# Performance work log

Hardware: AMD Instinct MI355X
Metric: run time of the kernel (lower is better)

The kernel has to match this reference:

```python
import jax, jax.numpy as jnp
import numpy as np
import math

B, S, HID, NH, INTER, L = 8, 512, 768, 12, 3072, 4
DH = HID // NH
EPS = 1e-12


def setup_inputs() -> dict:
    key = jax.random.key(0)
    ks = jax.random.split(key, 12)
    s = 0.02
    hidden_states = jax.random.normal(ks[0], (B, S, HID), jnp.float32)
    lengths = jax.random.randint(ks[1], (B,), S // 2, S + 1)
    attention_mask = (jnp.arange(S)[None, :] < lengths[:, None]).astype(jnp.float32)
    return dict(
        hidden_states=hidden_states,
        attention_mask=attention_mask,
        Wqkv_w=jax.random.normal(ks[2], (L, 3 * HID, HID), jnp.float32) * s,
        Wqkv_b=jnp.zeros((L, 3 * HID), jnp.float32),
        attn_out_w=jax.random.normal(ks[3], (L, HID, HID), jnp.float32) * s,
        attn_out_b=jnp.zeros((L, HID), jnp.float32),
        ln1_g=jnp.ones((L, HID), jnp.float32),
        ln1_b=jnp.zeros((L, HID), jnp.float32),
        glu_w=jax.random.normal(ks[4], (L, 2 * INTER, HID), jnp.float32) * s,
        wo_w=jax.random.normal(ks[5], (L, HID, INTER), jnp.float32) * s,
        wo_b=jnp.zeros((L, HID), jnp.float32),
        ln2_g=jnp.ones((L, HID), jnp.float32),
        ln2_b=jnp.zeros((L, HID), jnp.float32),
        r1=1.0 + 0.1 * jax.random.normal(ks[6], (L, NH, 1, 1), jnp.float32),
        r2=1.0 + 0.1 * jax.random.normal(ks[7], (L, NH, 1, 1), jnp.float32),
        r3=1.0 + 0.1 * jax.random.normal(ks[8], (L, NH, 1, 1), jnp.float32),
    )


def _ln(x, g, b):
    mu = x.mean(-1, keepdims=True)
    var = ((x - mu) ** 2).mean(-1, keepdims=True)
    return (x - mu) / jnp.sqrt(var + EPS) * g + b


def _forward(hidden_states, attention_mask, Wqkv_w, Wqkv_b, attn_out_w, attn_out_b,
             ln1_g, ln1_b, glu_w, wo_w, wo_b, ln2_g, ln2_b, r1, r2, r3):
    mask = attention_mask  # [B,S] float, 1=valid
    pos = jnp.arange(S)
    rel = jnp.abs(pos[None, :] - pos[:, None]).astype(jnp.float32)  # [S,S]
    rel_pos = rel > 0
    attn_bias = (1.0 - mask)[:, None, None, :] * -10000.0  # [B,1,1,S]
    # unpad_input <-> zero invalid rows of padded tensor
    h = hidden_states * mask[:, :, None]
    for l in range(L):
        c1 = jnp.clip(r1[l], 1e-7)  # [NH,1,1]
        c2 = jnp.clip(r2[l], 1e-7)
        c3 = jnp.clip(r3[l], 1e-7)
        relp = jnp.where(rel_pos, rel, 1.0) ** c3  # [NH,S,S], safe pow at |i-j|=0
        relp = jnp.where(rel_pos, relp, 0.0)
        kb = -c1 * jnp.log1p(c2 * relp)  # kerple bias [NH,S,S]
        bias = attn_bias + kb[None]  # [B,NH,S,S]
        # qkv on valid tokens only (pad_input reinserts zeros)
        qkv = (h @ Wqkv_w[l].T + Wqkv_b[l]) * mask[:, :, None]
        qkv = qkv.reshape(B, S, 3, NH, DH)
        q = qkv[:, :, 0].transpose(0, 2, 1, 3)  # [B,NH,S,DH]
        k = qkv[:, :, 1].transpose(0, 2, 1, 3)
        v = qkv[:, :, 2].transpose(0, 2, 1, 3)
        scores = jnp.einsum('bhqd,bhkd->bhqk', q, k) / math.sqrt(DH) + bias
        probs = jax.nn.softmax(scores, axis=-1)
        attn = jnp.einsum('bhqk,bhkd->bhqd', probs, v)
        attn = attn.transpose(0, 2, 1, 3).reshape(B, S, HID)
        ao = _ln(attn @ attn_out_w[l].T + attn_out_b[l] + h, ln1_g[l], ln1_b[l])
        ao = ao * mask[:, :, None]
        g = ao @ glu_w[l].T  # [B,S,2*INTER]
        x = jax.nn.gelu(g[..., :INTER], approximate=False) * g[..., INTER:]
        h = _ln(x @ wo_w[l].T + wo_b[l] + ao, ln2_g[l], ln2_b[l])
        h = h * mask[:, :, None]
    return h


def reference(hidden_states, attention_mask, Wqkv_w, Wqkv_b, attn_out_w, attn_out_b,
              ln1_g, ln1_b, glu_w, wo_w, wo_b, ln2_g, ln2_b, r1, r2, r3):
    return _forward(hidden_states, attention_mask, Wqkv_w, Wqkv_b, attn_out_w,
                    attn_out_b, ln1_g, ln1_b, glu_w, wo_w, wo_b, ln2_g, ln2_b,
                    r1, r2, r3)
```

## Files before the change

kernel.cpp:

```cpp
#include <hip/hip_runtime.h>
#include <hip/hip_bf16.h>
#include <math.h>

#define BQ 8
#define SQ 512
#define HID 768
#define NH 12
#define DH 64
#define INTER 3072
#define NL 4
#define M_TOK (BQ*SQ)

typedef unsigned short ushort_t;
typedef __attribute__((ext_vector_type(8))) short bf16x8;
typedef __attribute__((ext_vector_type(8))) unsigned short u16x8;
typedef __attribute__((ext_vector_type(4))) float f32x4;

__device__ __forceinline__ float bf2f(ushort_t u) {
  union { float f; unsigned int i; } v; v.i = ((unsigned int)u) << 16; return v.f;
}
__device__ __forceinline__ ushort_t f2bf(float f) {
  __hip_bfloat16 h = __float2bfloat16(f);
  return *reinterpret_cast<ushort_t*>(&h);
}

__device__ __forceinline__ void gload_lds16(const ushort_t* g, ushort_t* l) {
  __builtin_amdgcn_global_load_lds(
      (const __attribute__((address_space(1))) void*)g,
      (__attribute__((address_space(3))) void*)l, 16, 0, 0);
}

__global__ __launch_bounds__(256) void prep_kernel(
    const float* __restrict__ hidden, const float* __restrict__ amask,
    float* __restrict__ maskf, float* __restrict__ maskbias,
    float* __restrict__ h, ushort_t* __restrict__ hb)
{
  int i = blockIdx.x * 256 + threadIdx.x;
  if (i < M_TOK * HID) {
    float m = amask[i / HID];
    float v = hidden[i] * m;
    h[i] = v;
    hb[i] = f2bf(v);
    if (i < M_TOK) {
      maskf[i] = amask[i];
      maskbias[i] = (1.0f - amask[i]) * (-10000.0f);
    }
  }
}

__global__ void kerple_all_kernel(const float* __restrict__ r1,
                                  const float* __restrict__ r2,
                                  const float* __restrict__ r3,
                                  float* __restrict__ kbt_all)
{
  int lh = blockIdx.x;
  int d  = threadIdx.x;
  float c1 = fmaxf(r1[lh], 1e-7f);
  float c2 = fmaxf(r2[lh], 1e-7f);
  float c3 = fmaxf(r3[lh], 1e-7f);
  float v = 0.0f;
  if (d > 0) v = -c1 * log1pf(c2 * powf((float)d, c3));
  kbt_all[lh * SQ + d] = v;
}

#define WS0 (3*HID*HID)
#define WS1 (HID*HID)
#define WS2 (2*INTER*HID)
#define WS3 (HID*INTER)
#define WTOT (WS0+WS1+WS2+WS3)

__global__ __launch_bounds__(256) void wcast_layer_kernel(
    const float* __restrict__ w0, const float* __restrict__ w1,
    const float* __restrict__ w2, const float* __restrict__ w3,
    ushort_t* __restrict__ dst)
{
  int i = (blockIdx.x * 256 + threadIdx.x) * 4;
  if (i >= WTOT) return;
  const float* src; int off;
  if (i < WS0)                { src = w0; off = i; }
  else if (i < WS0+WS1)       { src = w1; off = i - WS0; }
  else if (i < WS0+WS1+WS2)   { src = w2; off = i - WS0 - WS1; }
  else                        { src = w3; off = i - WS0 - WS1 - WS2; }
  float4 v = *reinterpret_cast<const float4*>(src + off);
  ushort4 o;
  o.x = f2bf(v.x); o.y = f2bf(v.y); o.z = f2bf(v.z); o.w = f2bf(v.w);
  *reinterpret_cast<ushort4*>(dst + i) = o;
}

template<int NB, int EPI>
__global__ __launch_bounds__(256, 2) void mfma_gemm(
    const ushort_t* __restrict__ A, const ushort_t* __restrict__ B0p,
    const ushort_t* __restrict__ B1p, const float* __restrict__ bias,
    const float* __restrict__ rowscale, ushort_t* __restrict__ Cb,
    int N, int K)
{
  __shared__ ushort_t As_[128 * 64];
  __shared__ ushort_t Bs_[NB][128 * 64];
  int tid = threadIdx.x;
  int lane = tid & 63, w = tid >> 6;
  int wr = w >> 1, wc = w & 1;
  int bn = blockIdx.x, bm = blockIdx.y;

  f32x4 acc[NB][4][4];
#pragma unroll
  for (int p = 0; p < NB; ++p)
#pragma unroll
    for (int m = 0; m < 4; ++m)
#pragma unroll
      for (int n = 0; n < 4; ++n) acc[p][m][n] = (f32x4){0.f, 0.f, 0.f, 0.f};

  int sr[4], sc[4], so[4];
#pragma unroll
  for (int i = 0; i < 4; ++i) {
    int o = w * 4096 + i * 1024 + lane * 16;
    sr[i] = o >> 7;
    int cl = (o >> 4) & 7;
    sc[i] = cl ^ (sr[i] & 7);
    so[i] = (w * 4096 + i * 1024) >> 1;
  }
  const ushort_t* Arow  = A   + (size_t)bm * 128 * K;
  const ushort_t* Brow0 = B0p + (size_t)bn * 128 * K;
  const ushort_t* Brow1 = (NB == 2) ? (B1p + (size_t)bn * 128 * K) : nullptr;

  int aoff[4][2], boff[4][2];
#pragma unroll
  for (int m = 0; m < 4; ++m)
#pragma unroll
    for (int kh = 0; kh < 2; ++kh) {
      int ra = wr * 64 + m * 16 + (lane & 15);
      int rb = wc * 64 + m * 16 + (lane & 15);
      int ch = (kh * 4 + (lane >> 4)) ^ (lane & 7);
      aoff[m][kh] = ra * 64 + ch * 8;
      boff[m][kh] = rb * 64 + ch * 8;
    }

  for (int k0 = 0; k0 < K; k0 += 64) {
#pragma unroll
    for (int i = 0; i < 4; ++i)
      gload_lds16(Arow + (size_t)sr[i] * K + k0 + sc[i] * 8, As_ + so[i]);
#pragma unroll
    for (int i = 0; i < 4; ++i)
      gload_lds16(Brow0 + (size_t)sr[i] * K + k0 + sc[i] * 8, &Bs_[0][so[i]]);
    if constexpr (NB == 2) {
#pragma unroll
      for (int i = 0; i < 4; ++i)
        gload_lds16(Brow1 + (size_t)sr[i] * K + k0 + sc[i] * 8, &Bs_[1][so[i]]);
    }
    __syncthreads();
#pragma unroll
    for (int kh = 0; kh < 2; ++kh) {
      bf16x8 af[4], bf_[4];
#pragma unroll
      for (int m = 0; m < 4; ++m) af[m] = *(const bf16x8*)(As_ + aoff[m][kh]);
#pragma unroll
      for (int n = 0; n < 4; ++n) bf_[n] = *(const bf16x8*)(&Bs_[0][boff[n][kh]]);
#pragma unroll
      for (int m = 0; m < 4; ++m)
#pragma unroll
        for (int n = 0; n < 4; ++n)
          acc[0][m][n] = __builtin_amdgcn_mfma_f32_16x16x32_bf16(
              af[m], bf_[n], acc[0][m][n], 0, 0, 0);
      if constexpr (NB == 2) {
        bf16x8 bg[4];
#pragma unroll
        for (int n = 0; n < 4; ++n) bg[n] = *(const bf16x8*)(&Bs_[1][boff[n][kh]]);
#pragma unroll
        for (int m = 0; m < 4; ++m)
#pragma unroll
          for (int n = 0; n < 4; ++n)
            acc[1][m][n] = __builtin_amdgcn_mfma_f32_16x16x32_bf16(
                af[m], bg[n], acc[1][m][n], 0, 0, 0);
      }
    }
    __syncthreads();
  }

  int r0 = bm * 128 + wr * 64, c0 = bn * 128 + wc * 64;
#pragma unroll
  for (int m = 0; m < 4; ++m)
#pragma unroll
    for (int n = 0; n < 4; ++n) {
      int col  = c0 + n * 16 + (lane & 15);
      int rowb = r0 + m * 16 + (lane >> 4) * 4;
      if constexpr (EPI == 0) {
        float bv = bias ? bias[col] : 0.0f;
#pragma unroll
        for (int j = 0; j < 4; ++j)
          Cb[(size_t)(rowb + j) * N + col] = f2bf(acc[0][m][n][j] + bv);
      } else if constexpr (EPI == 1) {
#pragma unroll
        for (int j = 0; j < 4; ++j) {
          float va = acc[0][m][n][j];
          float vb = acc[1][m][n][j];
          float ge = 0.5f * va * (1.0f + erff(va * 0.70710678118654752440f));
          Cb[(size_t)(rowb + j) * N + col] = f2bf(ge * vb);
        }
      } else {
        float bv = bias ? bias[col] : 0.0f;
#pragma unroll
        for (int j = 0; j < 4; ++j) {
          float v = (acc[0][m][n][j] + bv) * rowscale[rowb + j];
          Cb[(size_t)(rowb + j) * N + col] = f2bf(v);
        }
      }
    }
}

__global__ __launch_bounds__(256) void attn_mfma(
    const ushort_t* __restrict__ qkvb, const float* __restrict__ kbt,
    const float* __restrict__ maskbias, ushort_t* __restrict__ attnb)
{
  __shared__ ushort_t Ks[64 * 64];
  __shared__ ushort_t Vt[64 * 64];
  __shared__ ushort_t Ps[64 * 64];
  __shared__ float    kbs[SQ];
  __shared__ float    mbs[SQ];

  int tid  = threadIdx.x;
  int lane = tid & 63, w = tid >> 6;
  int g = lane >> 4, r = lane & 15;
  int bid = blockIdx.x;
  int qt = bid & 7;
  int hh = (bid >> 3) % NH;
  int b  = bid / (8 * NH);
  int q0 = qt * 64;

  for (int i = tid; i < SQ; i += 256) {
    kbs[i] = kbt[hh * SQ + i];
    mbs[i] = maskbias[b * SQ + i];
  }

  bf16x8 qf[2];
  {
    const ushort_t* qsrc = qkvb + (size_t)(b * SQ + q0 + w * 16 + r) * (3 * HID)
                         + hh * DH + g * 8;
    qf[0] = *(const bf16x8*)(qsrc);
    qf[1] = *(const bf16x8*)(qsrc + 32);
  }

  float m_run[4], l_run[4];
  f32x4 oacc[4];
#pragma unroll
  for (int j = 0; j < 4; ++j) { m_run[j] = -1e30f; l_run[j] = 0.f; }
#pragma unroll
  for (int nd = 0; nd < 4; ++nd) oacc[nd] = (f32x4){0.f, 0.f, 0.f, 0.f};

  int k2 = (tid & 31) * 2, dg = tid >> 5;

  for (int kc = 0; kc < 8; ++kc) {
    __syncthreads();
#pragma unroll
    for (int ii = 0; ii < 2; ++ii) {
      int row = (w * 2 + ii) * 8 + (lane >> 3);
      int c   = lane & 7;
      const ushort_t* src = qkvb + (size_t)(b * SQ + kc * 64 + row) * (3 * HID)
                          + HID + hh * DH + ((c ^ (row & 7)) * 8);
      gload_lds16(src, Ks + (w * 2 + ii) * 512 + lane * 8);
    }
    {
      const ushort_t* v0 = qkvb + (size_t)(b * SQ + kc * 64 + k2) * (3 * HID)
                         + 2 * HID + hh * DH + dg * 8;
      const ushort_t* v1 = v0 + 3 * HID;
      u16x8 a = *(const u16x8*)v0;
      u16x8 c = *(const u16x8*)v1;
#pragma unroll
      for (int u = 0; u < 8; ++u) {
        int d = dg * 8 + u;
        int addr = d * 64 + (((k2 >> 3) ^ (d & 7)) * 8) + (k2 & 7);
        ushort2 pr; pr.x = (ushort_t)a[u]; pr.y = (ushort_t)c[u];
        *(ushort2*)(Vt + addr) = pr;
      }
    }
    __syncthreads();

    f32x4 sacc[4];
#pragma unroll
    for (int n = 0; n < 4; ++n) sacc[n] = (f32x4){0.f, 0.f, 0.f, 0.f};
    __builtin_amdgcn_s_setprio(1);
#pragma unroll
    for (int kh = 0; kh < 2; ++kh) {
#pragma unroll
      for (int n = 0; n < 4; ++n) {
        bf16x8 kf = *(const bf16x8*)(Ks + (n * 16 + r) * 64
                                     + (((g + kh * 4) ^ (r & 7)) * 8));
        sacc[n] = __builtin_amdgcn_mfma_f32_16x16x32_bf16(qf[kh], kf, sacc[n], 0, 0, 0);
      }
    }
    __builtin_amdgcn_s_setprio(0);

    float sval[4][4], mx[4];
#pragma unroll
    for (int j = 0; j < 4; ++j) mx[j] = -1e30f;
#pragma unroll
    for (int n = 0; n < 4; ++n) {
      int kg = kc * 64 + n * 16 + r;
      float mb = mbs[kg];
#pragma unroll
      for (int j = 0; j < 4; ++j) {
        int qg = q0 + w * 16 + g * 4 + j;
        float s = sacc[n][j] * 0.125f + mb + kbs[abs(qg - kg)];
        sval[n][j] = s;
        mx[j] = fmaxf(mx[j], s);
      }
    }
#pragma unroll
    for (int j = 0; j < 4; ++j) {
      mx[j] = fmaxf(mx[j], __shfl_xor(mx[j], 1));
      mx[j] = fmaxf(mx[j], __shfl_xor(mx[j], 2));
      mx[j] = fmaxf(mx[j], __shfl_xor(mx[j], 4));
      mx[j] = fmaxf(mx[j], __shfl_xor(mx[j], 8));
      float mn = fmaxf(m_run[j], mx[j]);
      mx[j] = __expf(m_run[j] - mn);
      m_run[j] = mn;
    }
    float rs[4] = {0.f, 0.f, 0.f, 0.f};
#pragma unroll
    for (int n = 0; n < 4; ++n) {
#pragma unroll
      for (int j = 0; j < 4; ++j) {
        float pp = __expf(sval[n][j] - m_run[j]);
        int prow = w * 16 + g * 4 + j;
        int pcol = n * 16 + r;
        Ps[prow * 64 + (((pcol >> 3) ^ (prow & 7)) * 8) + (pcol & 7)] = f2bf(pp);
        rs[j] += pp;
      }
    }
#pragma unroll
    for (int j = 0; j < 4; ++j) {
      rs[j] += __shfl_xor(rs[j], 1);
      rs[j] += __shfl_xor(rs[j], 2);
      rs[j] += __shfl_xor(rs[j], 4);
      rs[j] += __shfl_xor(rs[j], 8);
      l_run[j] = l_run[j] * mx[j] + rs[j];
    }
#pragma unroll
    for (int nd = 0; nd < 4; ++nd)
#pragma unroll
      for (int j = 0; j < 4; ++j) oacc[nd][j] *= mx[j];

    __builtin_amdgcn_s_setprio(1);
#pragma unroll
    for (int kh = 0; kh < 2; ++kh) {
      bf16x8 pa = *(const bf16x8*)(Ps + (w * 16 + r) * 64
                                   + (((g + kh * 4) ^ (r & 7)) * 8));
#pragma unroll
      for (int nd = 0; nd < 4; ++nd) {
        bf16x8 vf = *(const bf16x8*)(Vt + (nd * 16 + r) * 64
                                     + (((g + kh * 4) ^ (r & 7)) * 8));
        oacc[nd] = __builtin_amdgcn_mfma_f32_16x16x32_bf16(pa, vf, oacc[nd], 0, 0, 0);
      }
    }
    __builtin_amdgcn_s_setprio(0);
  }

#pragma unroll
  for (int j = 0; j < 4; ++j) {
    float inv = 1.0f / l_run[j];
    int token = b * SQ + q0 + w * 16 + g * 4 + j;
#pragma unroll
    for (int nd = 0; nd < 4; ++nd)
      attnb[(size_t)token * HID + hh * DH + nd * 16 + r] = f2bf(oacc[nd][j] * inv);
  }
}

__global__ __launch_bounds__(256) void ln_res_kernel(
    const ushort_t* __restrict__ t, const float* __restrict__ res,
    const float* __restrict__ g, const float* __restrict__ bb,
    const float* __restrict__ maskf, float* __restrict__ out,
    ushort_t* __restrict__ outb)
{
  __shared__ float part[8];
  int row = blockIdx.x, tid = threadIdx.x;
  int wid = tid >> 6;
  const ushort_t* tp = t + (size_t)row * HID;
  const float*    rp = res + (size_t)row * HID;
  float y0 = bf2f(tp[tid      ]) + rp[tid      ];
  float y1 = bf2f(tp[tid + 256]) + rp[tid + 256];
  float y2 = bf2f(tp[tid + 512]) + rp[tid + 512];

  float s = y0 + y1 + y2;
  s += __shfl_xor(s, 1);  s += __shfl_xor(s, 2);  s += __shfl_xor(s, 4);
  s += __shfl_xor(s, 8);  s += __shfl_xor(s, 16); s += __shfl_xor(s, 32);
  if ((tid & 63) == 0) part[wid] = s;
  __syncthreads();
  float mu = (part[0] + part[1] + part[2] + part[3]) * (1.0f / 768.0f);

  float d0 = y0 - mu, d1 = y1 - mu, d2 = y2 - mu;
  float v = d0*d0 + d1*d1 + d2*d2;
  v += __shfl_xor(v, 1);  v += __shfl_xor(v, 2);  v += __shfl_xor(v, 4);
  v += __shfl_xor(v, 8);  v += __shfl_xor(v, 16); v += __shfl_xor(v, 32);
  if ((tid & 63) == 0) part[4 + wid] = v;
  __syncthreads();
  float rstd = rsqrtf((part[4] + part[5] + part[6] + part[7]) * (1.0f / 768.0f)
                      + 1e-12f);
  float mk = maskf[row];
  float v0 = (d0*rstd*g[tid      ] + bb[tid      ]) * mk;
  float v1 = (d1*rstd*g[tid + 256] + bb[tid + 256]) * mk;
  float v2 = (d2*rstd*g[tid + 512] + bb[tid + 512]) * mk;
  size_t base = (size_t)row * HID;
  out[base + tid      ] = v0;  outb[base + tid      ] = f2bf(v0);
  out[base + tid + 256] = v1;  outb[base + tid + 256] = f2bf(v1);
  out[base + tid + 512] = v2;  outb[base + tid + 512] = f2bf(v2);
}

extern "C" void kernel_launch(void* const* d_in, const int* in_sizes, int n_in,
                              void* d_out, int out_size, void* d_ws, size_t ws_size,
                              hipStream_t stream) {
  const float* hidden     = (const float*)d_in[0];
  const float* amask      = (const float*)d_in[1];
  const float* Wqkv_w     = (const float*)d_in[2];
  const float* Wqkv_b     = (const float*)d_in[3];
  const float* attn_out_w = (const float*)d_in[4];
  const float* attn_out_b = (const float*)d_in[5];
  const float* ln1_g      = (const float*)d_in[6];
  const float* ln1_b      = (const float*)d_in[7];
  const float* glu_w      = (const float*)d_in[8];
  const float* wo_w       = (const float*)d_in[9];
  const float* wo_b       = (const float*)d_in[10];
  const float* ln2_g      = (const float*)d_in[11];
  const float* ln2_b      = (const float*)d_in[12];
  const float* r1         = (const float*)d_in[13];
  const float* r2         = (const float*)d_in[14];
  const float* r3         = (const float*)d_in[15];

  float* ws       = (float*)d_ws;
  float* maskf    = ws;
  float* maskbias = maskf    + 4096;
  float* kbt_all  = maskbias + 4096;
  float* h        = kbt_all  + NL*NH*SQ;
  float* ao       = h  + (size_t)M_TOK*HID;
  ushort_t* us    = (ushort_t*)(ao + (size_t)M_TOK*HID);
  ushort_t* hb    = us;
  ushort_t* aob   = hb    + (size_t)M_TOK*HID;
  ushort_t* atnb  = aob   + (size_t)M_TOK*HID;
  ushort_t* tb    = atnb  + (size_t)M_TOK*HID;
  ushort_t* qkv_b = tb    + (size_t)M_TOK*HID;
  ushort_t* xb    = qkv_b + (size_t)M_TOK*3*HID;
  ushort_t* wbf   = xb    + (size_t)M_TOK*INTER;

  prep_kernel<<<(M_TOK*HID + 255)/256, 256, 0, stream>>>(
      hidden, amask, maskf, maskbias, h, hb);
  kerple_all_kernel<<<NL*NH, SQ, 0, stream>>>(r1, r2, r3, kbt_all);

  for (int l = 0; l < NL; ++l) {
    wcast_layer_kernel<<<(WTOT/4 + 255)/256, 256, 0, stream>>>(
        Wqkv_w     + (size_t)l*WS0,
        attn_out_w + (size_t)l*WS1,
        glu_w      + (size_t)l*WS2,
        wo_w       + (size_t)l*WS3, wbf);
    ushort_t* wqkv = wbf;
    ushort_t* wao  = wbf + WS0;
    ushort_t* wga  = wbf + WS0 + WS1;
    ushort_t* wgb  = wga + (size_t)INTER*HID;
    ushort_t* wwo  = wbf + WS0 + WS1 + WS2;

    mfma_gemm<1,2><<<dim3(3*HID/128, M_TOK/128), 256, 0, stream>>>(
        hb, wqkv, nullptr, Wqkv_b + (size_t)l*3*HID, maskf, qkv_b, 3*HID, HID);

    attn_mfma<<<BQ*NH*8, 256, 0, stream>>>(
        qkv_b, kbt_all + (size_t)l*NH*SQ, maskbias, atnb);

    mfma_gemm<1,0><<<dim3(HID/128, M_TOK/128), 256, 0, stream>>>(
        atnb, wao, nullptr, attn_out_b + (size_t)l*HID, nullptr, tb, HID, HID);

    ln_res_kernel<<<M_TOK, 256, 0, stream>>>(tb, h, ln1_g + (size_t)l*HID,
                                             ln1_b + (size_t)l*HID, maskf, ao, aob);

    mfma_gemm<2,1><<<dim3(INTER/128, M_TOK/128), 256, 0, stream>>>(
        aob, wga, wgb, nullptr, nullptr, xb, INTER, HID);

    mfma_gemm<1,0><<<dim3(HID/128, M_TOK/128), 256, 0, stream>>>(
        xb, wwo, nullptr, wo_b + (size_t)l*HID, nullptr, tb, HID, INTER);

    float* hout = (l == NL - 1) ? (float*)d_out : h;
    ln_res_kernel<<<M_TOK, 256, 0, stream>>>(tb, ao, ln2_g + (size_t)l*HID,
                                             ln2_b + (size_t)l*HID, maskf, hout, hb);
  }
}
```

Before: 834.1 us.

## Double-buffer GEMM LDS tiles with async prefetch and per-GEMM tile shapes

Rewrites the MFMA GEMM to double-buffer the LDS tiles, issuing the next k-tile's global-to-LDS loads before computing the current one and waiting on a partial vmcnt, so memory latency overlaps compute. The kernel is templated on M-fragments, K-tile depth and wait count, and the launches pick a smaller 64-row M tile for the N=768 GEMMs to fill more blocks, and a 32-deep K tile for the dual-B GLU GEMM to fit LDS. The cost is a larger LDS footprint that may reduce occupancy. The hand-tuned vmcnt values must match the exact number of outstanding loads, or the kernel can read stale tiles.

```diff
diff --git a/kernel.cpp b/kernel.cpp
--- a/kernel.cpp
+++ b/kernel.cpp
@@ -28,6 +28,14 @@
   __builtin_amdgcn_global_load_lds(
       (const __attribute__((address_space(1))) void*)g,
       (__attribute__((address_space(3))) void*)l, 16, 0, 0);
+}
+
+template<int N>
+__device__ __forceinline__ void wait_vm() {
+  if constexpr (N == 0)      asm volatile("s_waitcnt vmcnt(0)" ::: "memory");
+  else if constexpr (N == 6) asm volatile("s_waitcnt vmcnt(6)" ::: "memory");
+  else if constexpr (N == 8) asm volatile("s_waitcnt vmcnt(8)" ::: "memory");
+  else                       asm volatile("s_waitcnt vmcnt(12)" ::: "memory");
 }
 
 __global__ __launch_bounds__(256) void prep_kernel(
@@ -87,75 +95,95 @@
   *reinterpret_cast<ushort4*>(dst + i) = o;
 }
 
-template<int NB, int EPI>
+template<int MF, int NB, int BK, int EPI, int VN>
 __global__ __launch_bounds__(256, 2) void mfma_gemm(
     const ushort_t* __restrict__ A, const ushort_t* __restrict__ B0p,
     const ushort_t* __restrict__ B1p, const float* __restrict__ bias,
     const float* __restrict__ rowscale, ushort_t* __restrict__ Cb,
     int N, int K)
 {
-  __shared__ ushort_t As_[128 * 64];
-  __shared__ ushort_t Bs_[NB][128 * 64];
+  constexpr int BM  = MF * 32;
+  constexpr int SMK = BK / 8 - 1;
+  constexpr int AIS = (BM * BK * 2) / 4096;
+  constexpr int BIS = (128 * BK * 2) / 4096;
+  constexpr int KH  = BK / 32;
+
+  __shared__ ushort_t As_[2][BM * BK];
+  __shared__ ushort_t Bs_[2][NB][128 * BK];
+
   int tid = threadIdx.x;
   int lane = tid & 63, w = tid >> 6;
   int wr = w >> 1, wc = w & 1;
+  int g = lane >> 4, r = lane & 15;
   int bn = blockIdx.x, bm = blockIdx.y;
 
-  f32x4 acc[NB][4][4];
+  f32x4 acc[NB][MF][4];
 #pragma unroll
   for (int p = 0; p < NB; ++p)
 #pragma unroll
-    for (int m = 0; m < 4; ++m)
+    for (int m = 0; m < MF; ++m)
 #pragma unroll
       for (int n = 0; n < 4; ++n) acc[p][m][n] = (f32x4){0.f, 0.f, 0.f, 0.f};
 
-  int sr[4], sc[4], so[4];
-#pragma unroll
-  for (int i = 0; i < 4; ++i) {
-    int o = w * 4096 + i * 1024 + lane * 16;
-    sr[i] = o >> 7;
-    int cl = (o >> 4) & 7;
-    sc[i] = cl ^ (sr[i] & 7);
-    so[i] = (w * 4096 + i * 1024) >> 1;
-  }
-  const ushort_t* Arow  = A   + (size_t)bm * 128 * K;
+  const ushort_t* Arow  = A   + (size_t)bm * BM * K;
   const ushort_t* Brow0 = B0p + (size_t)bn * 128 * K;
   const ushort_t* Brow1 = (NB == 2) ? (B1p + (size_t)bn * 128 * K) : nullptr;
 
-  int aoff[4][2], boff[4][2];
-#pragma unroll
-  for (int m = 0; m < 4; ++m)
-#pragma unroll
-    for (int kh = 0; kh < 2; ++kh) {
-      int ra = wr * 64 + m * 16 + (lane & 15);
-      int rb = wc * 64 + m * 16 + (lane & 15);
-      int ch = (kh * 4 + (lane >> 4)) ^ (lane & 7);
-      aoff[m][kh] = ra * 64 + ch * 8;
-      boff[m][kh] = rb * 64 + ch * 8;
-    }
-
-  for (int k0 = 0; k0 < K; k0 += 64) {
-#pragma unroll
-    for (int i = 0; i < 4; ++i)
-      gload_lds16(Arow + (size_t)sr[i] * K + k0 + sc[i] * 8, As_ + so[i]);
-#pragma unroll
-    for (int i = 0; i < 4; ++i)
-      gload_lds16(Brow0 + (size_t)sr[i] * K + k0 + sc[i] * 8, &Bs_[0][so[i]]);
-    if constexpr (NB == 2) {
-#pragma unroll
-      for (int i = 0; i < 4; ++i)
-        gload_lds16(Brow1 + (size_t)sr[i] * K + k0 + sc[i] * 8, &Bs_[1][so[i]]);
-    }
-    __syncthreads();
-#pragma unroll
-    for (int kh = 0; kh < 2; ++kh) {
-      bf16x8 af[4], bf_[4];
-#pragma unroll
-      for (int m = 0; m < 4; ++m) af[m] = *(const bf16x8*)(As_ + aoff[m][kh]);
-#pragma unroll
-      for (int n = 0; n < 4; ++n) bf_[n] = *(const bf16x8*)(&Bs_[0][boff[n][kh]]);
-#pragma unroll
-      for (int m = 0; m < 4; ++m)
+  auto stage = [&](const ushort_t* base, ushort_t* lds, int k0, int ISS_w) {
+#pragma unroll
+    for (int i = 0; i < 4; ++i) {
+      if (i >= ISS_w) break;
+      int o   = (w * ISS_w + i) * 1024 + lane * 16;
+      int row = o / (BK * 2);
+      int pc  = (o >> 4) & SMK;
+      int lc  = pc ^ (row & SMK);
+      gload_lds16(base + (size_t)row * K + k0 + lc * 8,
+                  lds + ((w * ISS_w + i) << 9));
+    }
+  };
+  auto stage_all = [&](int k0, int buf) {
+    stage(Arow,  &As_[buf][0],    k0, AIS);
+    stage(Brow0, &Bs_[buf][0][0], k0, BIS);
+    if constexpr (NB == 2) stage(Brow1, &Bs_[buf][1][0], k0, BIS);
+  };
+
+  int aoff[MF][KH], boff[4][KH];
+#pragma unroll
+  for (int m = 0; m < MF; ++m)
+#pragma unroll
+    for (int kh = 0; kh < KH; ++kh)
+      aoff[m][kh] = (wr * (BM/2) + m * 16 + r) * BK
+                  + (((kh * 4 + g) ^ (r & SMK)) * 8);
+#pragma unroll
+  for (int n = 0; n < 4; ++n)
+#pragma unroll
+    for (int kh = 0; kh < KH; ++kh)
+      boff[n][kh] = (wc * 64 + n * 16 + r) * BK
+                  + (((kh * 4 + g) ^ (r & SMK)) * 8);
+
+  int NT = K / BK;
+  stage_all(0, 0);
+
+  for (int t = 0; t < NT; ++t) {
+    int cur = t & 1;
+    if (t + 1 < NT) {
+      stage_all((t + 1) * BK, cur ^ 1);
+      wait_vm<VN>();
+    } else {
+      wait_vm<0>();
+    }
+    __builtin_amdgcn_s_barrier();
+
+    const ushort_t* Ab = &As_[cur][0];
+#pragma unroll
+    for (int kh = 0; kh < KH; ++kh) {
+      bf16x8 af[MF], bf_[4];
+#pragma unroll
+      for (int m = 0; m < MF; ++m) af[m] = *(const bf16x8*)(Ab + aoff[m][kh]);
+#pragma unroll
+      for (int n = 0; n < 4; ++n) bf_[n] = *(const bf16x8*)(&Bs_[cur][0][boff[n][kh]]);
+#pragma unroll
+      for (int m = 0; m < MF; ++m)
 #pragma unroll
         for (int n = 0; n < 4; ++n)
           acc[0][m][n] = __builtin_amdgcn_mfma_f32_16x16x32_bf16(
@@ -163,21 +191,21 @@
       if constexpr (NB == 2) {
         bf16x8 bg[4];
 #pragma unroll
-        for (int n = 0; n < 4; ++n) bg[n] = *(const bf16x8*)(&Bs_[1][boff[n][kh]]);
-#pragma unroll
-        for (int m = 0; m < 4; ++m)
+        for (int n = 0; n < 4; ++n) bg[n] = *(const bf16x8*)(&Bs_[cur][1][boff[n][kh]]);
+#pragma unroll
+        for (int m = 0; m < MF; ++m)
 #pragma unroll
           for (int n = 0; n < 4; ++n)
             acc[1][m][n] = __builtin_amdgcn_mfma_f32_16x16x32_bf16(
                 af[m], bg[n], acc[1][m][n], 0, 0, 0);
       }
     }
-    __syncthreads();
-  }
-
-  int r0 = bm * 128 + wr * 64, c0 = bn * 128 + wc * 64;
-#pragma unroll
-  for (int m = 0; m < 4; ++m)
+    __builtin_amdgcn_s_barrier();
+  }
+
+  int r0 = bm * BM + wr * (BM/2), c0 = bn * 128 + wc * 64;
+#pragma unroll
+  for (int m = 0; m < MF; ++m)
 #pragma unroll
     for (int n = 0; n < 4; ++n) {
       int col  = c0 + n * 16 + (lane & 15);
@@ -454,22 +482,22 @@
     ushort_t* wgb  = wga + (size_t)INTER*HID;
     ushort_t* wwo  = wbf + WS0 + WS1 + WS2;
 
-    mfma_gemm<1,2><<<dim3(3*HID/128, M_TOK/128), 256, 0, stream>>>(
+    mfma_gemm<4,1,64,2,8><<<dim3(3*HID/128, M_TOK/128), 256, 0, stream>>>(
         hb, wqkv, nullptr, Wqkv_b + (size_t)l*3*HID, maskf, qkv_b, 3*HID, HID);
 
     attn_mfma<<<BQ*NH*8, 256, 0, stream>>>(
         qkv_b, kbt_all + (size_t)l*NH*SQ, maskbias, atnb);
 
-    mfma_gemm<1,0><<<dim3(HID/128, M_TOK/128), 256, 0, stream>>>(
+    mfma_gemm<2,1,64,0,6><<<dim3(HID/128, M_TOK/64), 256, 0, stream>>>(
         atnb, wao, nullptr, attn_out_b + (size_t)l*HID, nullptr, tb, HID, HID);
 
     ln_res_kernel<<<M_TOK, 256, 0, stream>>>(tb, h, ln1_g + (size_t)l*HID,
                                              ln1_b + (size_t)l*HID, maskf, ao, aob);
 
-    mfma_gemm<2,1><<<dim3(INTER/128, M_TOK/128), 256, 0, stream>>>(
+    mfma_gemm<4,2,32,1,6><<<dim3(INTER/128, M_TOK/128), 256, 0, stream>>>(
         aob, wga, wgb, nullptr, nullptr, xb, INTER, HID);
 
-    mfma_gemm<1,0><<<dim3(HID/128, M_TOK/128), 256, 0, stream>>>(
+    mfma_gemm<2,1,64,0,6><<<dim3(HID/128, M_TOK/64), 256, 0, stream>>>(
         xb, wwo, nullptr, wo_b + (size_t)l*HID, nullptr, tb, HID, INTER);
 
     float* hout = (l == NL - 1) ? (float*)d_out : h;
```

After: 843.4 us. No clear change (+1.1%).
